# Performance work log

Measured on AMD Instinct MI355X. Metric: run time of the kernel, lower is better.

## Reference

```python
import jax, jax.numpy as jnp
import numpy as np
from jax import lax

B, N = 65536, 126  # batch, atoms (N % 3 == 0)


def _normalize(x):
    # matches torch.nn.functional.normalize(x, dim=-1): x / max(||x||, 1e-12)
    n = jnp.sqrt(jnp.sum(x * x, axis=-1, keepdims=True))
    return x / jnp.maximum(n, 1e-12)


def setup_inputs() -> dict:
    key = jax.random.key(0)
    k1, k2 = jax.random.split(key)
    angles = jax.random.normal(k1, (B, 2 * N), dtype=jnp.float32)
    prev_three = jax.random.normal(k2, (B, 3, 3), dtype=jnp.float32)
    return {"angles": angles, "prev_three": prev_three}


def _forward(angles, prev_three):
    Bb, L = angles.shape
    Nn = L // 2
    # chunk last dim into 2 halves, cat along dim 1, reshape, transpose -> (B, N, 2)
    ang = jnp.concatenate(jnp.split(angles, 2, axis=-1), axis=1)
    ang = ang.reshape(Bb, 2, Nn).transpose(0, 2, 1)
    sin_t = ang[..., 0]
    cos_t = ang[..., 1]
    n_t = jnp.sqrt(sin_t ** 2 + cos_t ** 2 + 1e-8)
    sin_t = sin_t / n_t
    cos_t = cos_t / n_t
    alpha = jnp.tile(jnp.array([2.028, 2.124, 1.941], dtype=angles.dtype), Nn // 3)  # (N,)
    bond = jnp.tile(jnp.array([1.329, 1.458, 1.523], dtype=angles.dtype), Nn // 3)   # (N,)
    sin_a = jnp.sin(alpha)[None, :]
    cos_a = jnp.broadcast_to(jnp.cos(alpha)[None, :], (Bb, Nn))
    rotation = jnp.stack([cos_a, sin_a * cos_t, -sin_a * sin_t], axis=2) * bond[None, :, None]  # (B,N,3)

    a0 = prev_three[:, 0, :]
    b0 = prev_three[:, 1, :]
    c0 = prev_three[:, 2, :]

    def step(carry, rot):
        # rot: (B, 3) for one atom
        a, b, c = carry
        bc = _normalize(b - c + 1e-8)
        n = _normalize(jnp.cross(b - a, bc) + 1e-8)
        m1 = jnp.cross(n, bc)
        d = c + rot[:, 0:1] * bc + rot[:, 1:2] * m1 + rot[:, 2:3] * n  # (B,3)
        return (b, c, d), d

    _, res = lax.scan(step, (a0, b0, c0), rotation.transpose(1, 0, 2))  # res: (N,B,3)
    return res.transpose(1, 0, 2)  # (B,N,3)


def reference(angles, prev_three):
    return _forward(angles, prev_three)
```

## Files before the change

### kernel.cpp

```cpp
#include <hip/hip_runtime.h>
#include <math.h>

#define NRES   126
#define CHUNK  21
#define NCHUNK (NRES / CHUNK)
#define ROWS   64
#define OUTF   (3 * CHUNK)

__device__ __forceinline__ float guarded_rsqrt(float x) {
    return __builtin_amdgcn_rsqf(fmaxf(x, 1e-24f));
}

__device__ __forceinline__ void nerf_step(
    float s, float co,
    float rc, float bs,
    float &ax, float &ay, float &az,
    float &bx, float &by, float &bz,
    float &cx, float &cy, float &cz,
    float &dx, float &dy, float &dz)
{
    float rnt = __builtin_amdgcn_rsqf(s * s + co * co + 1e-8f);
    s  *= rnt;
    co *= rnt;
    float r1 =  bs * co;
    float r2 = -(bs * s);

    float ux = bx - cx + 1e-8f;
    float uy = by - cy + 1e-8f;
    float uz = bz - cz + 1e-8f;
    float ru = guarded_rsqrt(ux * ux + uy * uy + uz * uz);
    ux *= ru; uy *= ru; uz *= ru;

    float vx = bx - ax;
    float vy = by - ay;
    float vz = bz - az;
    float nx = vy * uz - vz * uy + 1e-8f;
    float ny = vz * ux - vx * uz + 1e-8f;
    float nz = vx * uy - vy * ux + 1e-8f;
    float rn = guarded_rsqrt(nx * nx + ny * ny + nz * nz);
    nx *= rn; ny *= rn; nz *= rn;

    float mx = ny * uz - nz * uy;
    float my = nz * ux - nx * uz;
    float mz = nx * uy - ny * ux;

    dx = cx + rc * ux + r1 * mx + r2 * nx;
    dy = cy + rc * uy + r1 * my + r2 * ny;
    dz = cz + rc * uz + r1 * mz + r2 * nz;

    ax = bx; ay = by; az = bz;
    bx = cx; by = cy; bz = cz;
    cx = dx; cy = dy; cz = dz;
}

__global__ __launch_bounds__(ROWS, 1) void DihedralToCartesian_kernel(
    const float* __restrict__ angles,
    const float* __restrict__ prev,
    float* __restrict__ out,
    int nrows)
{
    __shared__ float s_sin[ROWS * CHUNK];
    __shared__ float s_cos[ROWS * CHUNK];
    __shared__ float s_out[ROWS * OUTF];

    const int t   = threadIdx.x;
    const int b0  = blockIdx.x * ROWS;
    const int row = b0 + t;

    const float* pr = prev + (size_t)row * 9;
    float ax = pr[0], ay = pr[1], az = pr[2];
    float bx = pr[3], by = pr[4], bz = pr[5];
    float cx = pr[6], cy = pr[7], cz = pr[8];

    const float rc0 = 1.329f * cosf(2.028f), bs0 = 1.329f * sinf(2.028f);
    const float rc1 = 1.458f * cosf(2.124f), bs1 = 1.458f * sinf(2.124f);
    const float rc2 = 1.523f * cosf(1.941f), bs2 = 1.523f * sinf(1.941f);

    float As[CHUNK], Ac[CHUNK];
    #pragma unroll
    for (int p = 0; p < CHUNK; ++p) {
        int idx = p * ROWS + t;
        int r   = idx / CHUNK;
        int j   = idx - r * CHUNK;
        const float* g = angles + (size_t)(b0 + r) * (2 * NRES);
        As[p] = g[j];
        Ac[p] = g[NRES + j];
    }

    for (int k = 0; k < NCHUNK; ++k) {
        const int i0 = k * CHUNK;

        __syncthreads();

        #pragma unroll
        for (int p = 0; p < CHUNK; ++p) {
            s_sin[p * ROWS + t] = As[p];
            s_cos[p * ROWS + t] = Ac[p];
        }

        __syncthreads();

        if (k + 1 < NCHUNK) {
            const int i0n = i0 + CHUNK;
            #pragma unroll
            for (int p = 0; p < CHUNK; ++p) {
                int idx = p * ROWS + t;
                int r   = idx / CHUNK;
                int j   = idx - r * CHUNK;
                const float* g = angles + (size_t)(b0 + r) * (2 * NRES) + i0n;
                As[p] = g[j];
                Ac[p] = g[NRES + j];
            }
        }

        float o[OUTF];
        float dx, dy, dz;
        #pragma unroll
        for (int j = 0; j < CHUNK; ++j) {
            float s  = s_sin[t * CHUNK + j];
            float co = s_cos[t * CHUNK + j];
            const int ph = j % 3;
            const float rc = (ph == 0) ? rc0 : (ph == 1) ? rc1 : rc2;
            const float bs = (ph == 0) ? bs0 : (ph == 1) ? bs1 : bs2;
            nerf_step(s, co, rc, bs, ax, ay, az, bx, by, bz, cx, cy, cz, dx, dy, dz);
            o[3 * j + 0] = dx;
            o[3 * j + 1] = dy;
            o[3 * j + 2] = dz;
        }

        #pragma unroll
        for (int q = 0; q < OUTF; ++q)
            s_out[t * OUTF + q] = o[q];

        __syncthreads();

        #pragma unroll
        for (int p = 0; p < OUTF; ++p) {
            int idx = p * ROWS + t;
            int r   = idx / OUTF;
            int jj  = idx - r * OUTF;
            out[(size_t)(b0 + r) * (3 * NRES) + (size_t)i0 * 3 + jj] = s_out[idx];
        }
    }
}

extern "C" void kernel_launch(void* const* d_in, const int* in_sizes, int n_in,
                              void* d_out, int out_size, void* d_ws, size_t ws_size,
                              hipStream_t stream)
{
    const float* angles = (const float*)d_in[0];
    const float* prev   = (const float*)d_in[1];
    float*       out    = (float*)d_out;

    int nrows = in_sizes[1] / 9;
    int grid  = nrows / ROWS;

    DihedralToCartesian_kernel<<<grid, ROWS, 0, stream>>>(angles, prev, out, nrows);
}
```

Before: 176.3 us.

## Stage angle chunks via direct global-to-LDS loads with double buffering

Replaces the register-staged angle prefetch with global_load_lds DMA into double-buffered shared memory, issued two chunks ahead. Block-wide barriers become manual s_waitcnt vmcnt/lgkmcnt waits, which is only sound because the block is a single 64-thread wavefront. The output store index math is replaced with incremental pointer updates. The aim is to cut register pressure and barrier overhead and to overlap loads with the serial NeRF compute. In exchange it depends on hardcoded vmcnt counts and wave-size assumptions.

```diff
diff --git a/kernel.cpp b/kernel.cpp
--- a/kernel.cpp
+++ b/kernel.cpp
@@ -3,17 +3,28 @@
 
 #define NRES   126
 #define CHUNK  21
-#define NCHUNK (NRES / CHUNK)
+#define NCHUNK 6
 #define ROWS   64
-#define OUTF   (3 * CHUNK)
+#define OUTF   63
+#define ISSUES 21
+
+#define LGKM0()   asm volatile("s_waitcnt lgkmcnt(0)" ::: "memory")
+#define VMWAIT42() asm volatile("s_waitcnt vmcnt(42)" ::: "memory")
+#define VM0()     asm volatile("s_waitcnt vmcnt(0)" ::: "memory")
+
+__device__ __forceinline__ void dma4(const float* g, float* l) {
+    __builtin_amdgcn_global_load_lds(
+        (const __attribute__((address_space(1))) void*)(g),
+        (__attribute__((address_space(3))) void*)(l),
+        4, 0, 0);
+}
 
 __device__ __forceinline__ float guarded_rsqrt(float x) {
     return __builtin_amdgcn_rsqf(fmaxf(x, 1e-24f));
 }
 
 __device__ __forceinline__ void nerf_step(
-    float s, float co,
-    float rc, float bs,
+    float s, float co, float rc, float bs,
     float &ax, float &ay, float &az,
     float &bx, float &by, float &bz,
     float &cx, float &cy, float &cz,
@@ -59,66 +70,56 @@
     float* __restrict__ out,
     int nrows)
 {
-    __shared__ float s_sin[ROWS * CHUNK];
-    __shared__ float s_cos[ROWS * CHUNK];
+    __shared__ float s_sin[2][ROWS * CHUNK];
+    __shared__ float s_cos[2][ROWS * CHUNK];
     __shared__ float s_out[ROWS * OUTF];
 
-    const int t   = threadIdx.x;
-    const int b0  = blockIdx.x * ROWS;
-    const int row = b0 + t;
+    const int t  = threadIdx.x;
+    const int b0 = blockIdx.x * ROWS;
 
-    const float* pr = prev + (size_t)row * 9;
+    auto stage = [&](int c, int sl) {
+        int r0 = t / 21;
+        int j  = t - r0 * 21;
+        const float* gs = angles + (size_t)(b0 + r0) * 252 + c * 21 + j;
+        #pragma unroll
+        for (int i = 0; i < ISSUES; ++i) {
+            dma4(gs,       &s_sin[sl][i * 64]);
+            dma4(gs + 126, &s_cos[sl][i * 64]);
+            int carry = (j >= 20) ? 1 : 0;
+            j += 1 - carry * 21;
+            gs += 757 + carry * 231;
+        }
+    };
+
+    stage(0, 0);
+    stage(1, 1);
+
+    const float* pr = prev + (size_t)(b0 + t) * 9;
     float ax = pr[0], ay = pr[1], az = pr[2];
     float bx = pr[3], by = pr[4], bz = pr[5];
     float cx = pr[6], cy = pr[7], cz = pr[8];
+
+    VM0();
 
     const float rc0 = 1.329f * cosf(2.028f), bs0 = 1.329f * sinf(2.028f);
     const float rc1 = 1.458f * cosf(2.124f), bs1 = 1.458f * sinf(2.124f);
     const float rc2 = 1.523f * cosf(1.941f), bs2 = 1.523f * sinf(1.941f);
 
-    float As[CHUNK], Ac[CHUNK];
-    #pragma unroll
-    for (int p = 0; p < CHUNK; ++p) {
-        int idx = p * ROWS + t;
-        int r   = idx / CHUNK;
-        int j   = idx - r * CHUNK;
-        const float* g = angles + (size_t)(b0 + r) * (2 * NRES);
-        As[p] = g[j];
-        Ac[p] = g[NRES + j];
-    }
+    #pragma unroll 1
+    for (int k = 0; k < NCHUNK; ++k) {
+        const int sl = k & 1;
 
-    for (int k = 0; k < NCHUNK; ++k) {
-        const int i0 = k * CHUNK;
+        VMWAIT42();
 
-        __syncthreads();
-
-        #pragma unroll
-        for (int p = 0; p < CHUNK; ++p) {
-            s_sin[p * ROWS + t] = As[p];
-            s_cos[p * ROWS + t] = Ac[p];
-        }
-
-        __syncthreads();
-
-        if (k + 1 < NCHUNK) {
-            const int i0n = i0 + CHUNK;
-            #pragma unroll
-            for (int p = 0; p < CHUNK; ++p) {
-                int idx = p * ROWS + t;
-                int r   = idx / CHUNK;
-                int j   = idx - r * CHUNK;
-                const float* g = angles + (size_t)(b0 + r) * (2 * NRES) + i0n;
-                As[p] = g[j];
-                Ac[p] = g[NRES + j];
-            }
-        }
+        const float* ssin = &s_sin[sl][t * CHUNK];
+        const float* scos = &s_cos[sl][t * CHUNK];
 
         float o[OUTF];
         float dx, dy, dz;
         #pragma unroll
         for (int j = 0; j < CHUNK; ++j) {
-            float s  = s_sin[t * CHUNK + j];
-            float co = s_cos[t * CHUNK + j];
+            float s  = ssin[j];
+            float co = scos[j];
             const int ph = j % 3;
             const float rc = (ph == 0) ? rc0 : (ph == 1) ? rc1 : rc2;
             const float bs = (ph == 0) ? bs0 : (ph == 1) ? bs1 : bs2;
@@ -132,15 +133,25 @@
         for (int q = 0; q < OUTF; ++q)
             s_out[t * OUTF + q] = o[q];
 
-        __syncthreads();
+        LGKM0();
 
-        #pragma unroll
-        for (int p = 0; p < OUTF; ++p) {
-            int idx = p * ROWS + t;
-            int r   = idx / OUTF;
-            int jj  = idx - r * OUTF;
-            out[(size_t)(b0 + r) * (3 * NRES) + (size_t)i0 * 3 + jj] = s_out[idx];
+        {
+            int r0  = (t >= 63) ? 1 : 0;
+            int jj  = t - r0 * 63;
+            float* op = out + (size_t)b0 * 378 + (size_t)k * 63 + (size_t)r0 * 378 + jj;
+            #pragma unroll
+            for (int p = 0; p < OUTF; ++p) {
+                op[0] = s_out[p * 64 + t];
+                int carry = (jj >= 62) ? 1 : 0;
+                jj += 1 - carry * 63;
+                op += 379 + carry * 315;
+            }
         }
+
+        LGKM0();
+
+        if (k + 2 < NCHUNK)
+            stage(k + 2, sl);
     }
 }
 
```

Result: slower. 185.3 us (+5.1%).
